# Kernel tuning notes

Hardware: AMD Instinct MI355X
Metric: run time of the kernel (lower is better)

The kernel has to match this reference:

```python
import jax, jax.numpy as jnp
import numpy as np

N_NODES = 50000
N_EDGES = 1600000
D_IN = 128
D_OUT = 32
ALPHA = 0.2  # LeakyReLU negative slope


def setup_inputs() -> dict:
    key = jax.random.key(0)
    k1, k2, k3, k4, k5, k6 = jax.random.split(key, 6)
    gain = float(np.sqrt(2.0))  # relu gain, xavier_normal-style scale
    X = jax.random.normal(k1, (N_NODES, D_IN), dtype=jnp.float32)
    weights = jax.random.normal(k2, (D_IN, D_OUT), dtype=jnp.float32) * (gain * np.sqrt(2.0 / (D_IN + D_OUT)))
    a0 = jax.random.normal(k3, (1, D_OUT), dtype=jnp.float32) * (gain * np.sqrt(2.0 / (1 + D_OUT)))
    a1 = jax.random.normal(k4, (1, D_OUT), dtype=jnp.float32) * (gain * np.sqrt(2.0 / (1 + D_OUT)))
    row_idx = jax.random.randint(k5, (N_EDGES,), 0, N_NODES, dtype=jnp.int32)
    col_idx = jax.random.randint(k6, (N_EDGES,), 0, N_NODES, dtype=jnp.int32)
    return {"X": X, "weights": weights, "a0": a0, "a1": a1,
            "row_idx": row_idx, "col_idx": col_idx}


def _minmax_norm(v):
    vmin = jnp.min(v)
    vmax = jnp.max(v)
    return (v - vmin) / (vmax - vmin)


def reference(X, weights, a0, a1, row_idx, col_idx):
    # X_prime = X @ W  -> [N, D]
    X_prime = X @ weights
    # Per-node partial scores; edge score e(i->j) = a0.X_prime[i] + a1.X_prime[j]
    s0 = jnp.sum(X_prime * a0, axis=-1)  # [N]
    s1 = jnp.sum(X_prime * a1, axis=-1)  # [N]
    att = s0[row_idx] + s1[col_idx]      # [E]
    # leakyrelu -> min-max normalize over all edges -> exp
    att = jax.nn.leaky_relu(att, negative_slope=ALPHA)
    att = jnp.exp(_minmax_norm(att))
    # rows_sum = SpMM(att, ones) = per-destination-row sum of edge weights
    rows_sum = jax.ops.segment_sum(att, row_idx, num_segments=N_NODES)  # [N]
    # h_prime = SpMM(att, X_prime) / rows_sum  (dropout p=0 -> identity)
    h = jax.ops.segment_sum(att[:, None] * X_prime[col_idx], row_idx,
                            num_segments=N_NODES)  # [N, D]
    return h / rows_sum[:, None]
```

## Files before the change

### kernel.cpp

```cpp
#include <hip/hip_runtime.h>
#include <hip/hip_bf16.h>
#include <math.h>

#define N_NODES 50000
#define N_EDGES 1600000
#define D_IN 128
#define D_OUT 32
#define ALPHA 0.2f

#define NB   512
#define RPB  98
#define HRPB 49
#define CAP  4096
#define CAPH 2048
#define PT   16
#define PBK  256
#define EB   (PT * PBK)
#define XNPB 32
#define NXB  ((N_NODES + XNPB - 1) / XNPB)
#define NPB  ((N_EDGES + EB - 1) / EB)
#define SNPB 32

__device__ __forceinline__ int enc_f(float x) {
    int i = __float_as_int(x);
    return i >= 0 ? i : (i ^ 0x7fffffff);
}
__device__ __forceinline__ float dec_f(int k) {
    return __int_as_float(k >= 0 ? k : (k ^ 0x7fffffff));
}
__device__ __forceinline__ unsigned short f2bf(float x) {
    __hip_bfloat16 h = __float2bfloat16(x);
    return *(unsigned short*)&h;
}
__device__ __forceinline__ float bf2f(unsigned short u) {
    return __uint_as_float((unsigned)u << 16);
}

__global__ __launch_bounds__(256) void k_s(const float* __restrict__ X,
                                           const float* __restrict__ W,
                                           const float* __restrict__ a0,
                                           const float* __restrict__ a1,
                                           float* __restrict__ s0,
                                           float* __restrict__ s1,
                                           int* __restrict__ minmax,
                                           int* __restrict__ gcount) {
    __shared__ float wa0[D_IN], wa1[D_IN];
    const int tid = threadIdx.x;
    if (blockIdx.x == 0) {
        if (tid == 0) {
            minmax[0] = 0x7fffffff;
            minmax[1] = (int)0x80000000;
        }
        for (int i = tid; i < NB; i += 256) gcount[i] = 0;
    }
    {
        const int k = tid & 127;
        const float4* Wr = (const float4*)(W + k * D_OUT);
        const float4* A = (const float4*)((tid < 128) ? a0 : a1);
        float acc = 0.f;
#pragma unroll
        for (int j = 0; j < 8; ++j) {
            const float4 w = Wr[j];
            const float4 a = A[j];
            acc += w.x * a.x + w.y * a.y + w.z * a.z + w.w * a.w;
        }
        if (tid < 128) wa0[k] = acc; else wa1[k] = acc;
    }
    __syncthreads();
    const int node = blockIdx.x * SNPB + (tid >> 3);
    const int l = tid & 7;
    if (node < N_NODES) {
        const float4* xr = (const float4*)(X + (size_t)node * D_IN) + l * 4;
        const float4* p4 = (const float4*)wa0 + l * 4;
        const float4* q4 = (const float4*)wa1 + l * 4;
        float v0 = 0.f, v1 = 0.f;
#pragma unroll
        for (int j = 0; j < 4; ++j) {
            const float4 x = xr[j];
            const float4 p = p4[j];
            const float4 q = q4[j];
            v0 += x.x * p.x + x.y * p.y + x.z * p.z + x.w * p.w;
            v1 += x.x * q.x + x.y * q.y + x.z * q.z + x.w * q.w;
        }
#pragma unroll
        for (int m = 4; m >= 1; m >>= 1) {
            v0 += __shfl_xor(v0, m);
            v1 += __shfl_xor(v1, m);
        }
        if (l == 0) { s0[node] = v0; s1[node] = v1; }
    }
}

__global__ __launch_bounds__(256) void k_fused(const float* __restrict__ X,
                                               const float* __restrict__ W,
                                               const int* __restrict__ row,
                                               const int* __restrict__ col,
                                               const float* __restrict__ s0,
                                               const float* __restrict__ s1,
                                               unsigned short* __restrict__ Xpb,
                                               int* __restrict__ minmax,
                                               int* __restrict__ gcount,
                                               uint2* __restrict__ gEdges) {
    __shared__ char smem[32768] __attribute__((aligned(16)));
    const int tid = threadIdx.x;
    if (blockIdx.x < NXB) {
        float4* Wl4 = (float4*)smem;
        float4* Xl4 = (float4*)(smem + 16384);
        const int node0 = blockIdx.x * XNPB;
        {
            const float4* W4 = (const float4*)W;
#pragma unroll
            for (int i = 0; i < 4; ++i) Wl4[tid + 256 * i] = W4[tid + 256 * i];
            const float4* X4 = (const float4*)X + (size_t)node0 * (D_IN / 4);
            const int lim = (min(XNPB, N_NODES - node0)) * (D_IN / 4);
#pragma unroll
            for (int i = 0; i < 4; ++i) {
                const int idx = tid + 256 * i;
                Xl4[idx] = (idx < lim) ? X4[idx] : make_float4(0.f, 0.f, 0.f, 0.f);
            }
        }
        __syncthreads();
        const int g = tid >> 3;
        const int l = tid & 7;
        const int node = node0 + g;
        const float4* xr = &Xl4[g * (D_IN / 4)];
        float ax = 0.f, ay = 0.f, az = 0.f, aw = 0.f;
#pragma unroll 4
        for (int kk = 0; kk < D_IN / 4; ++kk) {
            const float4 xv = xr[kk];
            const float4 w0 = Wl4[(4 * kk + 0) * 8 + l];
            const float4 w1 = Wl4[(4 * kk + 1) * 8 + l];
            const float4 w2 = Wl4[(4 * kk + 2) * 8 + l];
            const float4 w3 = Wl4[(4 * kk + 3) * 8 + l];
            ax += xv.x * w0.x + xv.y * w1.x + xv.z * w2.x + xv.w * w3.x;
            ay += xv.x * w0.y + xv.y * w1.y + xv.z * w2.y + xv.w * w3.y;
            az += xv.x * w0.z + xv.y * w1.z + xv.z * w2.z + xv.w * w3.z;
            aw += xv.x * w0.w + xv.y * w1.w + xv.z * w2.w + xv.w * w3.w;
        }
        if (node < N_NODES) {
            uint2 pk;
            pk.x = ((unsigned)f2bf(ay) << 16) | f2bf(ax);
            pk.y = ((unsigned)f2bf(aw) << 16) | f2bf(az);
            ((uint2*)Xpb)[(size_t)node * 8 + l] = pk;
        }
    } else {
        int* hist = (int*)smem;
        int* lcur = (int*)(smem + 2048);
        int* smn  = (int*)(smem + 4096);
        int* smx  = (int*)(smem + 4160);
        const int bb = blockIdx.x - NXB;
        for (int i = tid; i < NB; i += PBK) hist[i] = 0;
        __syncthreads();
        const int base = bb * EB;
        unsigned px[PT];
        float    fa[PT];
        int cnt = 0;
        int kmin = 0x7fffffff, kmax = 0x80000000;
        if (base + EB <= N_EDGES) {
#pragma unroll
            for (int i = 0; i < PT / 4; ++i) {
                const int4 r4 = ((const int4*)(row + base))[tid + i * PBK];
                const int4 c4 = ((const int4*)(col + base))[tid + i * PBK];
                const int rr[4] = {r4.x, r4.y, r4.z, r4.w};
                const int cc[4] = {c4.x, c4.y, c4.z, c4.w};
#pragma unroll
                for (int j = 0; j < 4; ++j) {
                    const int r = rr[j];
                    const int c = cc[j];
                    float a = s0[r] + s1[c];
                    a = a > 0.f ? a : ALPHA * a;
                    const int k = enc_f(a);
                    kmin = min(kmin, k);
                    kmax = max(kmax, k);
                    const unsigned b = (unsigned)r / RPB;
                    const unsigned lr = (unsigned)r - b * RPB;
                    px[cnt] = (b << 23) | (lr << 16) | (unsigned)c;
                    fa[cnt] = a;
                    ++cnt;
                    atomicAdd(&hist[b], 1);
                }
            }
        } else {
#pragma unroll
            for (int i = 0; i < PT; ++i) {
                const int e = base + i * PBK + tid;
                if (e >= N_EDGES) break;
                const int r = row[e];
                const int c = col[e];
                float a = s0[r] + s1[c];
                a = a > 0.f ? a : ALPHA * a;
                const int k = enc_f(a);
                kmin = min(kmin, k);
                kmax = max(kmax, k);
                const unsigned b = (unsigned)r / RPB;
                const unsigned lr = (unsigned)r - b * RPB;
                px[cnt] = (b << 23) | (lr << 16) | (unsigned)c;
                fa[cnt] = a;
                ++cnt;
                atomicAdd(&hist[b], 1);
            }
        }
        __syncthreads();
        for (int i = tid; i < NB; i += PBK) {
            const int h = hist[i];
            lcur[i] = h > 0 ? atomicAdd(&gcount[i], h) : 0;
        }
        __syncthreads();
        for (int j = 0; j < cnt; ++j) {
            const unsigned p = px[j];
            const unsigned b = p >> 23;
            const int pos = atomicAdd(&lcur[b], 1);
            if (pos < CAP)
                gEdges[(size_t)b * CAP + pos] =
                    make_uint2(p & 0x7FFFFFu, (unsigned)__float_as_int(fa[j]));
        }
#pragma unroll
        for (int m = 32; m >= 1; m >>= 1) {
            kmin = min(kmin, __shfl_xor(kmin, m));
            kmax = max(kmax, __shfl_xor(kmax, m));
        }
        const int wave = tid >> 6;
        if ((tid & 63) == 0) { smn[wave] = kmin; smx[wave] = kmax; }
        __syncthreads();
        if (tid == 0) {
#pragma unroll
            for (int w = 1; w < 4; ++w) {
                kmin = min(kmin, smn[w]);
                kmax = max(kmax, smx[w]);
            }
            atomicMin(&minmax[0], kmin);
            atomicMax(&minmax[1], kmax);
        }
    }
}

__global__ __launch_bounds__(512, 8) void k_bucket(const int* __restrict__ gcount,
                                                   const uint2* __restrict__ gEdges,
                                                   const unsigned short* __restrict__ Xpb,
                                                   const int* __restrict__ minmax,
                                                   float* __restrict__ out) {
    __shared__ unsigned short scol[CAPH];
    __shared__ float swt[CAPH];
    __shared__ int off[HRPB + 1];
    __shared__ int cur[HRPB];
    const int bid = blockIdx.x;
    const int b = bid >> 1;
    const int lo = (bid & 1) * HRPB;
    const int t = threadIdx.x;
    const float mn = dec_f(minmax[0]);
    const float mx = dec_f(minmax[1]);
    const float inv = 1.0f / (mx - mn);
    const int cnt = min(gcount[b], CAP);
    const uint2* eb = gEdges + (size_t)b * CAP;

    if (t < HRPB) cur[t] = 0;
    __syncthreads();
    for (int i = t; i < cnt; i += 512) {
        const int lrl = (int)(eb[i].x >> 16) - lo;
        if ((unsigned)lrl < (unsigned)HRPB) atomicAdd(&cur[lrl], 1);
    }
    __syncthreads();
    if (t == 0) {
        int run = 0;
#pragma unroll
        for (int r = 0; r < HRPB; ++r) { off[r] = run; run += cur[r]; }
        off[HRPB] = run;
    }
    __syncthreads();
    if (t < HRPB) cur[t] = off[t];
    __syncthreads();
    for (int i = t; i < cnt; i += 512) {
        const uint2 e = eb[i];
        const int lrl = (int)(e.x >> 16) - lo;
        if ((unsigned)lrl < (unsigned)HRPB) {
            const int p = atomicAdd(&cur[lrl], 1);
            if (p < CAPH) {
                scol[p] = (unsigned short)(e.x & 0xFFFFu);
                swt[p] = __expf((__int_as_float(e.y) - mn) * inv);
            }
        }
    }
    __syncthreads();

    const int proc = t >> 5;
    const int d = t & 31;
    for (int lrl = proc; lrl < HRPB; lrl += 16) {
        const int s = min(off[lrl], CAPH);
        const int e2 = min(off[lrl + 1], CAPH);
        float ac0 = 0.f, ac1 = 0.f, ac2 = 0.f, ac3 = 0.f;
        float w0s = 0.f, w1s = 0.f, w2s = 0.f, w3s = 0.f;
        int i = s;
        for (; i + 3 < e2; i += 4) {
            const int c0 = scol[i];
            const int c1 = scol[i + 1];
            const int c2 = scol[i + 2];
            const int c3 = scol[i + 3];
            const float w0 = swt[i];
            const float w1 = swt[i + 1];
            const float w2 = swt[i + 2];
            const float w3 = swt[i + 3];
            ac0 += w0 * bf2f(Xpb[(size_t)c0 * D_OUT + d]);
            ac1 += w1 * bf2f(Xpb[(size_t)c1 * D_OUT + d]);
            ac2 += w2 * bf2f(Xpb[(size_t)c2 * D_OUT + d]);
            ac3 += w3 * bf2f(Xpb[(size_t)c3 * D_OUT + d]);
            w0s += w0; w1s += w1; w2s += w2; w3s += w3;
        }
        for (; i < e2; ++i) {
            const float w0 = swt[i];
            ac0 += w0 * bf2f(Xpb[(size_t)scol[i] * D_OUT + d]);
            w0s += w0;
        }
        const int r = b * RPB + lo + lrl;
        if (r < N_NODES)
            out[(size_t)r * D_OUT + d] =
                (ac0 + ac1 + ac2 + ac3) / (w0s + w1s + w2s + w3s);
    }
}

extern "C" void kernel_launch(void* const* d_in, const int* in_sizes, int n_in,
                              void* d_out, int out_size, void* d_ws, size_t ws_size,
                              hipStream_t stream) {
    const float* X  = (const float*)d_in[0];
    const float* W  = (const float*)d_in[1];
    const float* a0 = (const float*)d_in[2];
    const float* a1 = (const float*)d_in[3];
    const int* row  = (const int*)d_in[4];
    const int* col  = (const int*)d_in[5];
    float* out = (float*)d_out;

    float* ws = (float*)d_ws;
    int*   minmax = (int*)ws;
    int*   gcount = (int*)(ws + 64);
    float* s0 = ws + 64 + 2048;
    float* s1 = s0 + 50048;
    unsigned short* Xpb = (unsigned short*)(s1 + 50048);
    uint2* gEdges = (uint2*)(s1 + 50048 + 800000);

    k_s<<<(N_NODES + SNPB - 1) / SNPB, 256, 0, stream>>>(X, W, a0, a1, s0, s1,
                                                         minmax, gcount);
    k_fused<<<NXB + NPB, 256, 0, stream>>>(X, W, row, col, s0, s1, Xpb,
                                           minmax, gcount, gEdges);
    k_bucket<<<NB * 2, 512, 0, stream>>>(gcount, gEdges, Xpb, minmax, out);
}
```

Measured before the change: 155.9 us.

## Fold score computation into GEMM kernel, split edge pass, shrink buckets, pack gathers

The score kernel is merged into the X@W kernel, so s0/s1 come from the projected rows held in registers and X is read only once. The edge-bucketing pass becomes its own kernel with 1021 buckets of 49 rows, which removes the half-bucket filtering in the aggregation kernel. Aggregation now has 16 threads per row, each gathering packed bf16 pairs as 32-bit loads, with float2 stores. The shared X tile is padded to avoid bank conflicts. In exchange, GEMM and edge work no longer overlap inside one launch, and the edge pass must wait for the GEMM kernel.

```diff
diff --git a/kernel.cpp b/kernel.cpp
--- a/kernel.cpp
+++ b/kernel.cpp
@@ -8,18 +8,17 @@
 #define D_OUT 32
 #define ALPHA 0.2f
 
-#define NB   512
-#define RPB  98
-#define HRPB 49
-#define CAP  4096
-#define CAPH 2048
-#define PT   16
+#define NB   1021
+#define NBP  1024
+#define RPB  49
+#define CAP  2048
+#define PT   8
 #define PBK  256
 #define EB   (PT * PBK)
+#define NPB  ((N_EDGES + EB - 1) / EB)
 #define XNPB 32
 #define NXB  ((N_NODES + XNPB - 1) / XNPB)
-#define NPB  ((N_EDGES + EB - 1) / EB)
-#define SNPB 32
+#define XLS  33
 
 __device__ __forceinline__ int enc_f(float x) {
     int i = __float_as_int(x);
@@ -36,52 +35,67 @@
     return __uint_as_float((unsigned)u << 16);
 }
 
-__global__ __launch_bounds__(256) void k_s(const float* __restrict__ X,
-                                           const float* __restrict__ W,
-                                           const float* __restrict__ a0,
-                                           const float* __restrict__ a1,
-                                           float* __restrict__ s0,
-                                           float* __restrict__ s1,
-                                           int* __restrict__ minmax,
-                                           int* __restrict__ gcount) {
-    __shared__ float wa0[D_IN], wa1[D_IN];
+__global__ __launch_bounds__(256) void k_gemm(const float* __restrict__ X,
+                                              const float* __restrict__ W,
+                                              const float* __restrict__ a0,
+                                              const float* __restrict__ a1,
+                                              unsigned short* __restrict__ Xpb,
+                                              float* __restrict__ s0,
+                                              float* __restrict__ s1,
+                                              int* __restrict__ minmax,
+                                              int* __restrict__ gcount) {
+    __shared__ float4 Wl4[1024];
+    __shared__ float4 Xl4[XNPB * XLS];
     const int tid = threadIdx.x;
     if (blockIdx.x == 0) {
         if (tid == 0) {
             minmax[0] = 0x7fffffff;
             minmax[1] = (int)0x80000000;
         }
-        for (int i = tid; i < NB; i += 256) gcount[i] = 0;
-    }
+        for (int i = tid; i < NBP; i += 256) gcount[i] = 0;
+    }
+    const int node0 = blockIdx.x * XNPB;
     {
-        const int k = tid & 127;
-        const float4* Wr = (const float4*)(W + k * D_OUT);
-        const float4* A = (const float4*)((tid < 128) ? a0 : a1);
-        float acc = 0.f;
-#pragma unroll
-        for (int j = 0; j < 8; ++j) {
-            const float4 w = Wr[j];
-            const float4 a = A[j];
-            acc += w.x * a.x + w.y * a.y + w.z * a.z + w.w * a.w;
-        }
-        if (tid < 128) wa0[k] = acc; else wa1[k] = acc;
-    }
-    __syncthreads();
-    const int node = blockIdx.x * SNPB + (tid >> 3);
+        const float4* W4 = (const float4*)W;
+#pragma unroll
+        for (int i = 0; i < 4; ++i) Wl4[tid + 256 * i] = W4[tid + 256 * i];
+        const float4* X4 = (const float4*)X + (size_t)node0 * (D_IN / 4);
+        const int lim = (min(XNPB, N_NODES - node0)) * (D_IN / 4);
+#pragma unroll
+        for (int i = 0; i < 4; ++i) {
+            const int idx = tid + 256 * i;
+            const float4 v = (idx < lim) ? X4[idx]
+                                         : make_float4(0.f, 0.f, 0.f, 0.f);
+            Xl4[(idx >> 5) * XLS + (idx & 31)] = v;
+        }
+    }
+    __syncthreads();
+    const int g = tid >> 3;
     const int l = tid & 7;
+    const int node = node0 + g;
+    const float4* xr = &Xl4[g * XLS];
+    float ax = 0.f, ay = 0.f, az = 0.f, aw = 0.f;
+#pragma unroll 4
+    for (int kk = 0; kk < D_IN / 4; ++kk) {
+        const float4 xv = xr[kk];
+        const float4 w0 = Wl4[(4 * kk + 0) * 8 + l];
+        const float4 w1 = Wl4[(4 * kk + 1) * 8 + l];
+        const float4 w2 = Wl4[(4 * kk + 2) * 8 + l];
+        const float4 w3 = Wl4[(4 * kk + 3) * 8 + l];
+        ax += xv.x * w0.x + xv.y * w1.x + xv.z * w2.x + xv.w * w3.x;
+        ay += xv.x * w0.y + xv.y * w1.y + xv.z * w2.y + xv.w * w3.y;
+        az += xv.x * w0.z + xv.y * w1.z + xv.z * w2.z + xv.w * w3.z;
+        aw += xv.x * w0.w + xv.y * w1.w + xv.z * w2.w + xv.w * w3.w;
+    }
     if (node < N_NODES) {
-        const float4* xr = (const float4*)(X + (size_t)node * D_IN) + l * 4;
-        const float4* p4 = (const float4*)wa0 + l * 4;
-        const float4* q4 = (const float4*)wa1 + l * 4;
-        float v0 = 0.f, v1 = 0.f;
-#pragma unroll
-        for (int j = 0; j < 4; ++j) {
-            const float4 x = xr[j];
-            const float4 p = p4[j];
-            const float4 q = q4[j];
-            v0 += x.x * p.x + x.y * p.y + x.z * p.z + x.w * p.w;
-            v1 += x.x * q.x + x.y * q.y + x.z * q.z + x.w * q.w;
-        }
+        uint2 pk;
+        pk.x = ((unsigned)f2bf(ay) << 16) | f2bf(ax);
+        pk.y = ((unsigned)f2bf(aw) << 16) | f2bf(az);
+        ((uint2*)Xpb)[(size_t)node * 8 + l] = pk;
+        const float4 av0 = ((const float4*)a0)[l];
+        const float4 av1 = ((const float4*)a1)[l];
+        float v0 = ax * av0.x + ay * av0.y + az * av0.z + aw * av0.w;
+        float v1 = ax * av1.x + ay * av1.y + az * av1.z + aw * av1.w;
 #pragma unroll
         for (int m = 4; m >= 1; m >>= 1) {
             v0 += __shfl_xor(v0, m);
@@ -91,102 +105,35 @@
     }
 }
 
-__global__ __launch_bounds__(256) void k_fused(const float* __restrict__ X,
-                                               const float* __restrict__ W,
-                                               const int* __restrict__ row,
-                                               const int* __restrict__ col,
-                                               const float* __restrict__ s0,
-                                               const float* __restrict__ s1,
-                                               unsigned short* __restrict__ Xpb,
-                                               int* __restrict__ minmax,
-                                               int* __restrict__ gcount,
-                                               uint2* __restrict__ gEdges) {
-    __shared__ char smem[32768] __attribute__((aligned(16)));
+__global__ __launch_bounds__(256) void k_edge(const int* __restrict__ row,
+                                              const int* __restrict__ col,
+                                              const float* __restrict__ s0,
+                                              const float* __restrict__ s1,
+                                              int* __restrict__ minmax,
+                                              int* __restrict__ gcount,
+                                              uint2* __restrict__ gEdges) {
+    __shared__ int hist[NBP];
+    __shared__ int lcur[NBP];
+    __shared__ int smn[4], smx[4];
     const int tid = threadIdx.x;
-    if (blockIdx.x < NXB) {
-        float4* Wl4 = (float4*)smem;
-        float4* Xl4 = (float4*)(smem + 16384);
-        const int node0 = blockIdx.x * XNPB;
-        {
-            const float4* W4 = (const float4*)W;
-#pragma unroll
-            for (int i = 0; i < 4; ++i) Wl4[tid + 256 * i] = W4[tid + 256 * i];
-            const float4* X4 = (const float4*)X + (size_t)node0 * (D_IN / 4);
-            const int lim = (min(XNPB, N_NODES - node0)) * (D_IN / 4);
-#pragma unroll
-            for (int i = 0; i < 4; ++i) {
-                const int idx = tid + 256 * i;
-                Xl4[idx] = (idx < lim) ? X4[idx] : make_float4(0.f, 0.f, 0.f, 0.f);
-            }
-        }
-        __syncthreads();
-        const int g = tid >> 3;
-        const int l = tid & 7;
-        const int node = node0 + g;
-        const float4* xr = &Xl4[g * (D_IN / 4)];
-        float ax = 0.f, ay = 0.f, az = 0.f, aw = 0.f;
-#pragma unroll 4
-        for (int kk = 0; kk < D_IN / 4; ++kk) {
-            const float4 xv = xr[kk];
-            const float4 w0 = Wl4[(4 * kk + 0) * 8 + l];
-            const float4 w1 = Wl4[(4 * kk + 1) * 8 + l];
-            const float4 w2 = Wl4[(4 * kk + 2) * 8 + l];
-            const float4 w3 = Wl4[(4 * kk + 3) * 8 + l];
-            ax += xv.x * w0.x + xv.y * w1.x + xv.z * w2.x + xv.w * w3.x;
-            ay += xv.x * w0.y + xv.y * w1.y + xv.z * w2.y + xv.w * w3.y;
-            az += xv.x * w0.z + xv.y * w1.z + xv.z * w2.z + xv.w * w3.z;
-            aw += xv.x * w0.w + xv.y * w1.w + xv.z * w2.w + xv.w * w3.w;
-        }
-        if (node < N_NODES) {
-            uint2 pk;
-            pk.x = ((unsigned)f2bf(ay) << 16) | f2bf(ax);
-            pk.y = ((unsigned)f2bf(aw) << 16) | f2bf(az);
-            ((uint2*)Xpb)[(size_t)node * 8 + l] = pk;
-        }
-    } else {
-        int* hist = (int*)smem;
-        int* lcur = (int*)(smem + 2048);
-        int* smn  = (int*)(smem + 4096);
-        int* smx  = (int*)(smem + 4160);
-        const int bb = blockIdx.x - NXB;
-        for (int i = tid; i < NB; i += PBK) hist[i] = 0;
-        __syncthreads();
-        const int base = bb * EB;
-        unsigned px[PT];
-        float    fa[PT];
-        int cnt = 0;
-        int kmin = 0x7fffffff, kmax = 0x80000000;
-        if (base + EB <= N_EDGES) {
-#pragma unroll
-            for (int i = 0; i < PT / 4; ++i) {
-                const int4 r4 = ((const int4*)(row + base))[tid + i * PBK];
-                const int4 c4 = ((const int4*)(col + base))[tid + i * PBK];
-                const int rr[4] = {r4.x, r4.y, r4.z, r4.w};
-                const int cc[4] = {c4.x, c4.y, c4.z, c4.w};
-#pragma unroll
-                for (int j = 0; j < 4; ++j) {
-                    const int r = rr[j];
-                    const int c = cc[j];
-                    float a = s0[r] + s1[c];
-                    a = a > 0.f ? a : ALPHA * a;
-                    const int k = enc_f(a);
-                    kmin = min(kmin, k);
-                    kmax = max(kmax, k);
-                    const unsigned b = (unsigned)r / RPB;
-                    const unsigned lr = (unsigned)r - b * RPB;
-                    px[cnt] = (b << 23) | (lr << 16) | (unsigned)c;
-                    fa[cnt] = a;
-                    ++cnt;
-                    atomicAdd(&hist[b], 1);
-                }
-            }
-        } else {
-#pragma unroll
-            for (int i = 0; i < PT; ++i) {
-                const int e = base + i * PBK + tid;
-                if (e >= N_EDGES) break;
-                const int r = row[e];
-                const int c = col[e];
+    for (int i = tid; i < NBP; i += PBK) hist[i] = 0;
+    __syncthreads();
+    const int base = blockIdx.x * EB;
+    unsigned px[PT];
+    float    fa[PT];
+    int cnt = 0;
+    int kmin = 0x7fffffff, kmax = 0x80000000;
+    if (base + EB <= N_EDGES) {
+#pragma unroll
+        for (int i = 0; i < PT / 4; ++i) {
+            const int4 r4 = ((const int4*)(row + base))[tid + i * PBK];
+            const int4 c4 = ((const int4*)(col + base))[tid + i * PBK];
+            const int rr[4] = {r4.x, r4.y, r4.z, r4.w};
+            const int cc[4] = {c4.x, c4.y, c4.z, c4.w};
+#pragma unroll
+            for (int j = 0; j < 4; ++j) {
+                const int r = rr[j];
+                const int c = cc[j];
                 float a = s0[r] + s1[c];
                 a = a > 0.f ? a : ALPHA * a;
                 const int k = enc_f(a);
@@ -194,43 +141,62 @@
                 kmax = max(kmax, k);
                 const unsigned b = (unsigned)r / RPB;
                 const unsigned lr = (unsigned)r - b * RPB;
-                px[cnt] = (b << 23) | (lr << 16) | (unsigned)c;
+                px[cnt] = (b << 22) | (lr << 16) | (unsigned)c;
                 fa[cnt] = a;
                 ++cnt;
                 atomicAdd(&hist[b], 1);
             }
         }
-        __syncthreads();
-        for (int i = tid; i < NB; i += PBK) {
-            const int h = hist[i];
-            lcur[i] = h > 0 ? atomicAdd(&gcount[i], h) : 0;
-        }
-        __syncthreads();
-        for (int j = 0; j < cnt; ++j) {
-            const unsigned p = px[j];
-            const unsigned b = p >> 23;
-            const int pos = atomicAdd(&lcur[b], 1);
-            if (pos < CAP)
-                gEdges[(size_t)b * CAP + pos] =
-                    make_uint2(p & 0x7FFFFFu, (unsigned)__float_as_int(fa[j]));
-        }
-#pragma unroll
-        for (int m = 32; m >= 1; m >>= 1) {
-            kmin = min(kmin, __shfl_xor(kmin, m));
-            kmax = max(kmax, __shfl_xor(kmax, m));
-        }
-        const int wave = tid >> 6;
-        if ((tid & 63) == 0) { smn[wave] = kmin; smx[wave] = kmax; }
-        __syncthreads();
-        if (tid == 0) {
-#pragma unroll
-            for (int w = 1; w < 4; ++w) {
-                kmin = min(kmin, smn[w]);
-                kmax = max(kmax, smx[w]);
-            }
-            atomicMin(&minmax[0], kmin);
-            atomicMax(&minmax[1], kmax);
-        }
+    } else {
+#pragma unroll
+        for (int i = 0; i < PT; ++i) {
+            const int e = base + i * PBK + tid;
+            if (e >= N_EDGES) break;
+            const int r = row[e];
+            const int c = col[e];
+            float a = s0[r] + s1[c];
+            a = a > 0.f ? a : ALPHA * a;
+            const int k = enc_f(a);
+            kmin = min(kmin, k);
+            kmax = max(kmax, k);
+            const unsigned b = (unsigned)r / RPB;
+            const unsigned lr = (unsigned)r - b * RPB;
+            px[cnt] = (b << 22) | (lr << 16) | (unsigned)c;
+            fa[cnt] = a;
+            ++cnt;
+            atomicAdd(&hist[b], 1);
+        }
+    }
+    __syncthreads();
+    for (int i = tid; i < NBP; i += PBK) {
+        const int h = hist[i];
+        lcur[i] = h > 0 ? atomicAdd(&gcount[i], h) : 0;
+    }
+    __syncthreads();
+    for (int j = 0; j < cnt; ++j) {
+        const unsigned p = px[j];
+        const unsigned b = p >> 22;
+        const int pos = atomicAdd(&lcur[b], 1);
+        if (pos < CAP)
+            gEdges[(size_t)b * CAP + pos] =
+                make_uint2(p & 0x3FFFFFu, (unsigned)__float_as_int(fa[j]));
+    }
+#pragma unroll
+    for (int m = 32; m >= 1; m >>= 1) {
+        kmin = min(kmin, __shfl_xor(kmin, m));
+        kmax = max(kmax, __shfl_xor(kmax, m));
+    }
+    const int wave = tid >> 6;
+    if ((tid & 63) == 0) { smn[wave] = kmin; smx[wave] = kmax; }
+    __syncthreads();
+    if (tid == 0) {
+#pragma unroll
+        for (int w = 1; w < 4; ++w) {
+            kmin = min(kmin, smn[w]);
+            kmax = max(kmax, smx[w]);
+        }
+        atomicMin(&minmax[0], kmin);
+        atomicMax(&minmax[1], kmax);
     }
 }
 
@@ -239,13 +205,11 @@
                                                    const unsigned short* __restrict__ Xpb,
                                                    const int* __restrict__ minmax,
                                                    float* __restrict__ out) {
-    __shared__ unsigned short scol[CAPH];
-    __shared__ float swt[CAPH];
-    __shared__ int off[HRPB + 1];
-    __shared__ int cur[HRPB];
-    const int bid = blockIdx.x;
-    const int b = bid >> 1;
-    const int lo = (bid & 1) * HRPB;
+    __shared__ unsigned short scol[CAP];
+    __shared__ float swt[CAP];
+    __shared__ int off[RPB + 1];
+    __shared__ int cur[RPB];
+    const int b = blockIdx.x;
     const int t = threadIdx.x;
     const float mn = dec_f(minmax[0]);
     const float mx = dec_f(minmax[1]);
@@ -253,41 +217,38 @@
     const int cnt = min(gcount[b], CAP);
     const uint2* eb = gEdges + (size_t)b * CAP;
 
-    if (t < HRPB) cur[t] = 0;
-    __syncthreads();
-    for (int i = t; i < cnt; i += 512) {
-        const int lrl = (int)(eb[i].x >> 16) - lo;
-        if ((unsigned)lrl < (unsigned)HRPB) atomicAdd(&cur[lrl], 1);
-    }
+    if (t < RPB) cur[t] = 0;
+    __syncthreads();
+    for (int i = t; i < cnt; i += 512) atomicAdd(&cur[eb[i].x >> 16], 1);
     __syncthreads();
     if (t == 0) {
         int run = 0;
 #pragma unroll
-        for (int r = 0; r < HRPB; ++r) { off[r] = run; run += cur[r]; }
-        off[HRPB] = run;
-    }
-    __syncthreads();
-    if (t < HRPB) cur[t] = off[t];
+        for (int r = 0; r < RPB; ++r) { off[r] = run; run += cur[r]; }
+        off[RPB] = run;
+    }
+    __syncthreads();
+    if (t < RPB) cur[t] = off[t];
     __syncthreads();
     for (int i = t; i < cnt; i += 512) {
         const uint2 e = eb[i];
-        const int lrl = (int)(e.x >> 16) - lo;
-        if ((unsigned)lrl < (unsigned)HRPB) {
-            const int p = atomicAdd(&cur[lrl], 1);
-            if (p < CAPH) {
-                scol[p] = (unsigned short)(e.x & 0xFFFFu);
-                swt[p] = __expf((__int_as_float(e.y) - mn) * inv);
-            }
-        }
-    }
-    __syncthreads();
-
-    const int proc = t >> 5;
-    const int d = t & 31;
-    for (int lrl = proc; lrl < HRPB; lrl += 16) {
-        const int s = min(off[lrl], CAPH);
-        const int e2 = min(off[lrl + 1], CAPH);
-        float ac0 = 0.f, ac1 = 0.f, ac2 = 0.f, ac3 = 0.f;
+        const int lr = (int)(e.x >> 16);
+        const int p = atomicAdd(&cur[lr], 1);
+        if (p < CAP) {
+            scol[p] = (unsigned short)(e.x & 0xFFFFu);
+            swt[p] = __expf((__int_as_float(e.y) - mn) * inv);
+        }
+    }
+    __syncthreads();
+
+    const int proc = t >> 4;
+    const int d2 = t & 15;
+    const unsigned* Xp32 = (const unsigned*)Xpb;
+    for (int lr = proc; lr < RPB; lr += 32) {
+        const int s = off[lr];
+        const int e2 = off[lr + 1];
+        float pa0 = 0.f, pa1 = 0.f, pa2 = 0.f, pa3 = 0.f;
+        float pb0 = 0.f, pb1 = 0.f, pb2 = 0.f, pb3 = 0.f;
         float w0s = 0.f, w1s = 0.f, w2s = 0.f, w3s = 0.f;
         int i = s;
         for (; i + 3 < e2; i += 4) {
@@ -299,21 +260,35 @@
             const float w1 = swt[i + 1];
             const float w2 = swt[i + 2];
             const float w3 = swt[i + 3];
-            ac0 += w0 * bf2f(Xpb[(size_t)c0 * D_OUT + d]);
-            ac1 += w1 * bf2f(Xpb[(size_t)c1 * D_OUT + d]);
-            ac2 += w2 * bf2f(Xpb[(size_t)c2 * D_OUT + d]);
-            ac3 += w3 * bf2f(Xpb[(size_t)c3 * D_OUT + d]);
+            const unsigned u0 = Xp32[(size_t)c0 * 16 + d2];
+            const unsigned u1 = Xp32[(size_t)c1 * 16 + d2];
+            const unsigned u2 = Xp32[(size_t)c2 * 16 + d2];
+            const unsigned u3 = Xp32[(size_t)c3 * 16 + d2];
+            pa0 += w0 * bf2f((unsigned short)(u0 & 0xFFFFu));
+            pb0 += w0 * bf2f((unsigned short)(u0 >> 16));
+            pa1 += w1 * bf2f((unsigned short)(u1 & 0xFFFFu));
+            pb1 += w1 * bf2f((unsigned short)(u1 >> 16));
+            pa2 += w2 * bf2f((unsigned short)(u2 & 0xFFFFu));
+            pb2 += w2 * bf2f((unsigned short)(u2 >> 16));
+            pa3 += w3 * bf2f((unsigned short)(u3 & 0xFFFFu));
+            pb3 += w3 * bf2f((unsigned short)(u3 >> 16));
             w0s += w0; w1s += w1; w2s += w2; w3s += w3;
         }
         for (; i < e2; ++i) {
-            const float w0 = swt[i];
-            ac0 += w0 * bf2f(Xpb[(size_t)scol[i] * D_OUT + d]);
-            w0s += w0;
-        }
-        const int r = b * RPB + lo + lrl;
-        if (r < N_NODES)
-            out[(size_t)r * D_OUT + d] =
-                (ac0 + ac1 + ac2 + ac3) / (w0s + w1s + w2s + w3s);
+            const float w = swt[i];
+            const unsigned u = Xp32[(size_t)scol[i] * 16 + d2];
+            pa0 += w * bf2f((unsigned short)(u & 0xFFFFu));
+            pb0 += w * bf2f((unsigned short)(u >> 16));
+            w0s += w;
+        }
+        const int r = b * RPB + lr;
+        if (r < N_NODES) {
+            const float ws = w0s + w1s + w2s + w3s;
+            float2 o;
+            o.x = (pa0 + pa1 + pa2 + pa3) / ws;
+            o.y = (pb0 + pb1 + pb2 + pb3) / ws;
+            ((float2*)out)[(size_t)r * 16 + d2] = o;
+        }
     }
 }
 
@@ -336,9 +311,7 @@
     unsigned short* Xpb = (unsigned short*)(s1 + 50048);
     uint2* gEdges = (uint2*)(s1 + 50048 + 800000);
 
-    k_s<<<(N_NODES + SNPB - 1) / SNPB, 256, 0, stream>>>(X, W, a0, a1, s0, s1,
-                                                         minmax, gcount);
-    k_fused<<<NXB + NPB, 256, 0, stream>>>(X, W, row, col, s0, s1, Xpb,
-                                           minmax, gcount, gEdges);
-    k_bucket<<<NB * 2, 512, 0, stream>>>(gcount, gEdges, Xpb, minmax, out);
-}
+    k_gemm<<<NXB, 256, 0, stream>>>(X, W, a0, a1, Xpb, s0, s1, minmax, gcount);
+    k_edge<<<NPB, 256, 0, stream>>>(row, col, s0, s1, minmax, gcount, gEdges);
+    k_bucket<<<NB, 512, 0, stream>>>(gcount, gEdges, Xpb, minmax, out);
+}
```

New measurement: 158.4 us. About the same (+1.6%).
